# Optimization experiments

Hardware: AMD Instinct MI355X
Metric: run time of the kernel (lower is better)

The kernel has to match this reference:

```python
import jax, jax.numpy as jnp
import numpy as np

N_NODES = 50000
N_EDGES = 800000
IN_FEAT = 256
OUT_FEAT = 256
NUM_RELS = 64
NUM_BASES = 8


def setup_inputs() -> dict:
    key = jax.random.key(0)
    ks = jax.random.split(key, 9)
    x = jax.random.normal(ks[0], (N_NODES, IN_FEAT), dtype=jnp.float32)
    src = jax.random.randint(ks[1], (N_EDGES,), 0, N_NODES, dtype=jnp.int32)
    dst = jax.random.randint(ks[2], (N_EDGES,), 0, N_NODES, dtype=jnp.int32)
    etypes = jax.random.randint(ks[3], (N_EDGES,), 0, NUM_RELS, dtype=jnp.int32)
    norm = jax.random.uniform(ks[4], (N_EDGES, 1), dtype=jnp.float32)
    # glorot-style params
    s_w = (6.0 / (IN_FEAT + OUT_FEAT)) ** 0.5
    weight = jax.random.uniform(ks[5], (NUM_BASES, IN_FEAT, OUT_FEAT), jnp.float32, -s_w, s_w)
    s_c = (6.0 / (NUM_RELS + NUM_BASES)) ** 0.5
    w_comp = jax.random.uniform(ks[6], (NUM_RELS, NUM_BASES), jnp.float32, -s_c, s_c)
    h_bias = jnp.zeros((OUT_FEAT,), jnp.float32)
    loop_weight = jax.random.uniform(ks[7], (IN_FEAT, OUT_FEAT), jnp.float32, -s_w, s_w)
    return {"x": x, "src": src, "dst": dst, "etypes": etypes, "norm": norm,
            "weight": weight, "w_comp": w_comp, "h_bias": h_bias,
            "loop_weight": loop_weight}


def reference(x, src, dst, etypes, norm, weight, w_comp, h_bias, loop_weight):
    # Basis regularizer with num_bases < num_rels:
    #   W_r = sum_b w_comp[r, b] * V_b
    # Per-edge message: msg_e = (x[src_e] @ W_{etype_e}) * norm_e,
    # aggregated by sum onto destination nodes. Since the map is linear,
    # we aggregate per basis first, then apply V_b (8 dense GEMMs).
    n_nodes = x.shape[0]
    coef = w_comp[etypes]                      # [E, B] per-edge basis coeffs
    xs = x[src] * norm                         # [E, D] normalized source feats
    out = jnp.zeros((n_nodes, weight.shape[2]), x.dtype)
    for b in range(weight.shape[0]):           # small fixed loop over bases
        agg = jax.ops.segment_sum(xs * coef[:, b:b + 1], dst,
                                  num_segments=n_nodes)   # [N, D]
        out = out + agg @ weight[b]            # [N, O]
    out = out + h_bias + x @ loop_weight       # bias + self-loop
    return jax.nn.relu(out)
```

## Files before the change

### kernel.cpp

```cpp
#include <hip/hip_runtime.h>
#include <hip/hip_bf16.h>
#include <stdint.h>

#define N_NODES 50000
#define N_EDGES 800000
#define IN_FEAT 256
#define OUT_FEAT 256
#define NUM_RELS 64
#define NUM_BASES 8
#define KTOT 2304
#define KAGG 2048
#define MP 50176
#define NT 36
#define SCAN_BLKS 196

typedef __attribute__((ext_vector_type(8))) __bf16 bf16x8;
typedef __attribute__((ext_vector_type(4))) __bf16 bf16x4;
typedef __attribute__((ext_vector_type(4))) float f32x4;
typedef __attribute__((ext_vector_type(2))) float f32x2;

static __device__ __forceinline__ void gload_lds16(const void* g, void* l) {
  auto gp = (const __attribute__((address_space(1))) void*)(uintptr_t)g;
  auto lp = (__attribute__((address_space(3))) void*)(uint32_t)(uintptr_t)l;
  __builtin_amdgcn_global_load_lds(gp, lp, 16, 0, 0);
}

__global__ void k_prex(const float* __restrict__ x, __bf16* __restrict__ xb) {
  int i = blockIdx.x * 256 + threadIdx.x;
  const float4* xp = (const float4*)x;
  float4 u = xp[i * 2], v = xp[i * 2 + 1];
  bf16x8 o;
  o[0] = (__bf16)u.x; o[1] = (__bf16)u.y; o[2] = (__bf16)u.z; o[3] = (__bf16)u.w;
  o[4] = (__bf16)v.x; o[5] = (__bf16)v.y; o[6] = (__bf16)v.z; o[7] = (__bf16)v.w;
  *(bf16x8*)(xb + (size_t)i * 8) = o;
}

__global__ void k_count(const int* __restrict__ dst, int* __restrict__ deg) {
  int e = blockIdx.x * 256 + threadIdx.x;
  atomicAdd(&deg[dst[e]], 1);
}

__global__ void k_scan1(const int* __restrict__ deg, int* __restrict__ offs,
                        int* __restrict__ bsum) {
  __shared__ int s[256];
  int t = threadIdx.x;
  int i = blockIdx.x * 256 + t;
  int v = (i < N_NODES) ? deg[i] : 0;
  s[t] = v;
  __syncthreads();
  for (int d = 1; d < 256; d <<= 1) {
    int y = (t >= d) ? s[t - d] : 0;
    __syncthreads();
    s[t] += y;
    __syncthreads();
  }
  if (i < N_NODES) offs[i] = s[t] - v;
  if (t == 255) bsum[blockIdx.x] = s[255];
}

__global__ void k_scan3(int* __restrict__ offs, const int* __restrict__ bsum,
                        int* __restrict__ fill) {
  __shared__ int s[256];
  int t = threadIdx.x;
  s[t] = (t < SCAN_BLKS && t < blockIdx.x) ? bsum[t] : 0;
  __syncthreads();
  for (int d = 128; d; d >>= 1) {
    if (t < d) s[t] += s[t + d];
    __syncthreads();
  }
  int base = s[0];
  int i = blockIdx.x * 256 + t;
  if (i < N_NODES) {
    int o = offs[i] + base;
    offs[i] = o;
    fill[i] = o;
  }
}

__global__ void k_scatter(const int* __restrict__ dst, const int* __restrict__ srcv,
                          const int* __restrict__ ety, const float* __restrict__ norm,
                          int* __restrict__ fill, uint2* __restrict__ erec) {
  int e = blockIdx.x * 256 + threadIdx.x;
  int pos = atomicAdd(&fill[dst[e]], 1);
  erec[pos] = make_uint2((unsigned)srcv[e] | ((unsigned)ety[e] << 16),
                         __float_as_uint(norm[e]));
}

#define AGGE(R, XV, ACC)                                                      \
  do {                                                                        \
    int et_ = __builtin_amdgcn_readfirstlane((int)((R).x >> 16));             \
    float nm_ = __uint_as_float((R).y);                                       \
    f32x2 v0_ = {__uint_as_float((XV).x << 16) * nm_,                         \
                 __uint_as_float((XV).x & 0xffff0000u) * nm_};                 \
    f32x2 v1_ = {__uint_as_float((XV).y << 16) * nm_,                         \
                 __uint_as_float((XV).y & 0xffff0000u) * nm_};                 \
    f32x4 cl_ = *(const f32x4*)(w_comp + et_ * 8);                            \
    f32x4 ch_ = *(const f32x4*)(w_comp + et_ * 8 + 4);                        \
    _Pragma("unroll") for (int b = 0; b < 4; ++b) {                           \
      ACC[b][0] += v0_ * cl_[b];                                              \
      ACC[b][1] += v1_ * cl_[b];                                              \
      ACC[b + 4][0] += v0_ * ch_[b];                                          \
      ACC[b + 4][1] += v1_ * ch_[b];                                          \
    }                                                                         \
  } while (0)

#define EDGE4(RP, I, ACC)                                                     \
  do {                                                                        \
    uint2 r0_ = (RP)[(I) + 0], r1_ = (RP)[(I) + 1];                           \
    uint2 r2_ = (RP)[(I) + 2], r3_ = (RP)[(I) + 3];                           \
    uint2 x0_ = *(const uint2*)(xb + (size_t)(r0_.x & 0xffffu) * IN_FEAT + lo4);\
    uint2 x1_ = *(const uint2*)(xb + (size_t)(r1_.x & 0xffffu) * IN_FEAT + lo4);\
    uint2 x2_ = *(const uint2*)(xb + (size_t)(r2_.x & 0xffffu) * IN_FEAT + lo4);\
    uint2 x3_ = *(const uint2*)(xb + (size_t)(r3_.x & 0xffffu) * IN_FEAT + lo4);\
    AGGE(r0_, x0_, ACC); AGGE(r1_, x1_, ACC);                                 \
    AGGE(r2_, x2_, ACC); AGGE(r3_, x3_, ACC);                                 \
  } while (0)

#define EDGE1(RP, I, ACC)                                                     \
  do {                                                                        \
    uint2 r_ = (RP)[(I)];                                                     \
    uint2 x_ = *(const uint2*)(xb + (size_t)(r_.x & 0xffffu) * IN_FEAT + lo4);\
    AGGE(r_, x_, ACC);                                                        \
  } while (0)

__global__ __launch_bounds__(256) void k_agg(
    const __bf16* __restrict__ xb, const float* __restrict__ w_comp,
    const int* __restrict__ offs, const int* __restrict__ fin,
    const uint2* __restrict__ erec, __bf16* __restrict__ A) {
  int t = threadIdx.x;
  int wid = t >> 6, lane = t & 63;
  int na = blockIdx.x * 8 + wid * 2;
  int lo4 = lane * 4;

  f32x2 acca[NUM_BASES][2], accb[NUM_BASES][2];
#pragma unroll
  for (int b = 0; b < NUM_BASES; ++b) {
    acca[b][0] = f32x2{0.f, 0.f}; acca[b][1] = f32x2{0.f, 0.f};
    accb[b][0] = f32x2{0.f, 0.f}; accb[b][1] = f32x2{0.f, 0.f};
  }

  int i0a = __builtin_amdgcn_readfirstlane(offs[na]);
  int ca  = __builtin_amdgcn_readfirstlane(fin[na]) - i0a;
  int i0b = __builtin_amdgcn_readfirstlane(offs[na + 1]);
  int cb  = __builtin_amdgcn_readfirstlane(fin[na + 1]) - i0b;
  const uint2* rpa = erec + i0a;
  const uint2* rpb = erec + i0b;

  int ia = 0, ib = 0;
  int mm = (ca < cb ? ca : cb) & ~3;
  for (; ia < mm; ia += 4, ib += 4) {
    EDGE4(rpa, ia, acca);
    EDGE4(rpb, ib, accb);
  }
  for (; ia + 4 <= ca; ia += 4) EDGE4(rpa, ia, acca);
  for (; ib + 4 <= cb; ib += 4) EDGE4(rpb, ib, accb);
  for (; ia < ca; ++ia) EDGE1(rpa, ia, acca);
  for (; ib < cb; ++ib) EDGE1(rpb, ib, accb);

  __bf16* Ara = A + (size_t)na * KAGG + lo4;
  __bf16* Arb = A + (size_t)(na + 1) * KAGG + lo4;
#pragma unroll
  for (int b = 0; b < NUM_BASES; ++b) {
    bf16x4 oa, ob;
    oa[0] = (__bf16)acca[b][0][0]; oa[1] = (__bf16)acca[b][0][1];
    oa[2] = (__bf16)acca[b][1][0]; oa[3] = (__bf16)acca[b][1][1];
    *(bf16x4*)(Ara + b * 256) = oa;
    ob[0] = (__bf16)accb[b][0][0]; ob[1] = (__bf16)accb[b][0][1];
    ob[2] = (__bf16)accb[b][1][0]; ob[3] = (__bf16)accb[b][1][1];
    *(bf16x4*)(Arb + b * 256) = ob;
  }
}

__global__ void k_prepwf(const float* __restrict__ weight, const float* __restrict__ loop_w,
                         __bf16* __restrict__ Wf) {
  int tid = blockIdx.x * 256 + threadIdx.x;
  int lane6 = tid & 63;
  int F = tid >> 6;
  int kt2 = F >> 4;
  int nf = F & 15;
  int o = nf * 16 + (lane6 & 15);
  int rbase = kt2 * 32 + (lane6 >> 4) * 8;
  bf16x8 v;
#pragma unroll
  for (int j = 0; j < 8; ++j) {
    int r = rbase + j;
    float f = (r < 2048) ? weight[(size_t)r * 256 + o]
                         : loop_w[(size_t)(r - 2048) * 256 + o];
    v[j] = (__bf16)f;
  }
  *(bf16x8*)(Wf + (size_t)tid * 8) = v;
}

__global__ __launch_bounds__(256, 2) void k_gemm(const __bf16* __restrict__ A,
                                                 const __bf16* __restrict__ xb,
                                                 const __bf16* __restrict__ Wf,
                                                 const float* __restrict__ bias,
                                                 float* __restrict__ out) {
  __shared__ __align__(16) __bf16 sA[3 * 64 * 64];

  int t = threadIdx.x;
  int wid = t >> 6, lane = t & 63;
  int tm = blockIdx.x;
  int rfw = __builtin_amdgcn_readfirstlane(wid);

  f32x4 acc[4][4];
#pragma unroll
  for (int m = 0; m < 4; ++m)
#pragma unroll
    for (int n = 0; n < 4; ++n) acc[m][n] = f32x4{0.f, 0.f, 0.f, 0.f};

  int frow = lane & 15;
  int g = lane >> 4;
  int f7 = frow & 7;
  int kb0 = ((g ^ f7) << 4);
  int kb1 = (((4 + g) ^ f7) << 4);

  int rh = t >> 3;
  int qoff = ((t & 7) ^ (rh & 7)) * 8;
  const __bf16* gA[2];
  const __bf16* gX[2];
#pragma unroll
  for (int it = 0; it < 2; ++it) {
    int row = it * 32 + rh;
    gA[it] = A + (size_t)(tm * 64 + row) * KAGG + qoff;
    gX[it] = xb + (size_t)(tm * 64 + row) * IN_FEAT + qoff;
  }
  const __bf16* wfb = Wf + (size_t)(wid * 4) * 512 + lane * 8;

  bf16x8 af[4][2], B0[4][2], B1[4][2];

#define VMWAIT(N) asm volatile("s_waitcnt vmcnt(" #N ")" ::: "memory")
#define BAR()                                       \
  do {                                              \
    asm volatile("" ::: "memory");                  \
    __builtin_amdgcn_s_barrier();                   \
    asm volatile("" ::: "memory");                  \
  } while (0)

#define STAGE(U, BUF)                                                         \
  do {                                                                        \
    char* d_ = (char*)sA + (BUF) * 8192;                                      \
    if ((U) < 32) {                                                           \
      int ko_ = (U) * 64;                                                     \
      gload_lds16(gA[0] + ko_, d_ + rfw * 1024);                              \
      gload_lds16(gA[1] + ko_, d_ + 4096 + rfw * 1024);                       \
    } else {                                                                  \
      int ko_ = ((U) - 32) * 64;                                              \
      gload_lds16(gX[0] + ko_, d_ + rfw * 1024);                              \
      gload_lds16(gX[1] + ko_, d_ + 4096 + rfw * 1024);                       \
    }                                                                         \
  } while (0)

#define LOADB(KT, DST)                                                        \
  do {                                                                        \
    _Pragma("unroll") for (int nf = 0; nf < 4; ++nf) {                        \
      DST[nf][0] = *(const bf16x8*)(wfb + (size_t)(((KT) * 2 + 0) * 16 + nf) * 512); \
      DST[nf][1] = *(const bf16x8*)(wfb + (size_t)(((KT) * 2 + 1) * 16 + nf) * 512); \
    }                                                                         \
  } while (0)

#define READ_A(BUF)                                                           \
  do {                                                                        \
    const char* b_ = (const char*)sA + (BUF) * 8192;                          \
    _Pragma("unroll") for (int mf = 0; mf < 4; ++mf) {                        \
      int r_ = mf * 16 + frow;                                                \
      af[mf][0] = *(const bf16x8*)(b_ + r_ * 128 + kb0);                      \
      af[mf][1] = *(const bf16x8*)(b_ + r_ * 128 + kb1);                      \
    }                                                                         \
  } while (0)

#define MFMA32(BS)                                                            \
  do {                                                                        \
    _Pragma("unroll") for (int mf = 0; mf < 4; ++mf)                          \
    _Pragma("unroll") for (int nf = 0; nf < 4; ++nf) {                        \
      acc[mf][nf] = __builtin_amdgcn_mfma_f32_16x16x32_bf16(                  \
          af[mf][0], BS[nf][0], acc[mf][nf], 0, 0, 0);                        \
      acc[mf][nf] = __builtin_amdgcn_mfma_f32_16x16x32_bf16(                  \
          af[mf][1], BS[nf][1], acc[mf][nf], 0, 0, 0);                        \
    }                                                                         \
  } while (0)

#define STEP(KT, BCUR, BNXT)                                                  \
  do {                                                                        \
    int cb_ = (KT) % 3;                                                       \
    int nb_ = ((KT) + 2) % 3;                                                 \
    int u2_ = ((KT) + 2 < NT) ? (KT) + 2 : NT - 1;                            \
    int un_ = ((KT) + 1 < NT) ? (KT) + 1 : NT - 1;                            \
    LOADB(un_, BNXT);                                                         \
    STAGE(u2_, nb_);                                                          \
    READ_A(cb_);                                                              \
    __builtin_amdgcn_s_setprio(1);                                            \
    MFMA32(BCUR);                                                             \
    __builtin_amdgcn_s_setprio(0);                                            \
    VMWAIT(10);                                                               \
    BAR();                                                                    \
  } while (0)

  LOADB(0, B0);
  STAGE(0, 0);
  STAGE(1, 1);
  VMWAIT(2);
  BAR();

  for (int kt = 0; kt < NT; kt += 2) {
    STEP(kt, B0, B1);
    STEP(kt + 1, B1, B0);
  }
#undef STEP
#undef STAGE
#undef LOADB
#undef READ_A
#undef MFMA32
#undef VMWAIT
#undef BAR

  int r0 = (lane >> 4) * 4;
  int c0 = lane & 15;
#pragma unroll
  for (int m = 0; m < 4; ++m) {
    int rowb = tm * 64 + m * 16 + r0;
#pragma unroll
    for (int n = 0; n < 4; ++n) {
      int col = wid * 64 + n * 16 + c0;
      float bv = bias[col];
#pragma unroll
      for (int r = 0; r < 4; ++r) {
        int row = rowb + r;
        if (row < N_NODES) {
          float v = acc[m][n][r] + bv;
          out[(size_t)row * OUT_FEAT + col] = v > 0.f ? v : 0.f;
        }
      }
    }
  }
}

extern "C" void kernel_launch(void* const* d_in, const int* in_sizes, int n_in,
                              void* d_out, int out_size, void* d_ws, size_t ws_size,
                              hipStream_t stream) {
  const float* x      = (const float*)d_in[0];
  const int*   src    = (const int*)d_in[1];
  const int*   dst    = (const int*)d_in[2];
  const int*   ety    = (const int*)d_in[3];
  const float* norm   = (const float*)d_in[4];
  const float* weight = (const float*)d_in[5];
  const float* w_comp = (const float*)d_in[6];
  const float* h_bias = (const float*)d_in[7];
  const float* loop_w = (const float*)d_in[8];
  float* out = (float*)d_out;

  char* ws = (char*)d_ws;
  __bf16* A  = (__bf16*)ws;
  size_t off = (size_t)MP * KAGG * 2;
  __bf16* xb = (__bf16*)(ws + off);
  off += (size_t)MP * IN_FEAT * 2;
  __bf16* Wf = (__bf16*)(ws + off);
  off += (size_t)256 * KTOT * 2;
  uint2* erec = (uint2*)(ws + off);
  off += (size_t)N_EDGES * 8;
  int* deg   = (int*)(ws + off);
  int* offs  = deg + N_NODES;
  int* fill  = offs + N_NODES;
  int* bsum  = fill + N_NODES;

  hipMemsetAsync(deg, 0, N_NODES * sizeof(int), stream);
  k_prex<<<(N_NODES * IN_FEAT / 8) / 256, 256, 0, stream>>>(x, xb);
  k_count<<<N_EDGES / 256, 256, 0, stream>>>(dst, deg);
  k_scan1<<<SCAN_BLKS, 256, 0, stream>>>(deg, offs, bsum);
  k_scan3<<<SCAN_BLKS, 256, 0, stream>>>(offs, bsum, fill);
  k_scatter<<<N_EDGES / 256, 256, 0, stream>>>(dst, src, ety, norm, fill, erec);
  k_agg<<<N_NODES / 8, 256, 0, stream>>>(xb, w_comp, offs, fill, erec, A);
  k_prepwf<<<288, 256, 0, stream>>>(weight, loop_w, Wf);
  k_gemm<<<MP / 64, 256, 0, stream>>>(A, xb, Wf, h_bias, out);
}
```

Before: 299.9 us.

## Load GEMM A fragments directly from global memory into registers, dropping LDS staging

```diff
diff --git a/kernel.cpp b/kernel.cpp
--- a/kernel.cpp
+++ b/kernel.cpp
@@ -11,19 +11,12 @@
 #define KTOT 2304
 #define KAGG 2048
 #define MP 50176
-#define NT 36
 #define SCAN_BLKS 196
 
 typedef __attribute__((ext_vector_type(8))) __bf16 bf16x8;
 typedef __attribute__((ext_vector_type(4))) __bf16 bf16x4;
 typedef __attribute__((ext_vector_type(4))) float f32x4;
 typedef __attribute__((ext_vector_type(2))) float f32x2;
-
-static __device__ __forceinline__ void gload_lds16(const void* g, void* l) {
-  auto gp = (const __attribute__((address_space(1))) void*)(uintptr_t)g;
-  auto lp = (__attribute__((address_space(3))) void*)(uint32_t)(uintptr_t)l;
-  __builtin_amdgcn_global_load_lds(gp, lp, 16, 0, 0);
-}
 
 __global__ void k_prex(const float* __restrict__ x, __bf16* __restrict__ xb) {
   int i = blockIdx.x * 256 + threadIdx.x;
@@ -196,123 +189,76 @@
                                                  const __bf16* __restrict__ Wf,
                                                  const float* __restrict__ bias,
                                                  float* __restrict__ out) {
-  __shared__ __align__(16) __bf16 sA[3 * 64 * 64];
-
   int t = threadIdx.x;
   int wid = t >> 6, lane = t & 63;
   int tm = blockIdx.x;
-  int rfw = __builtin_amdgcn_readfirstlane(wid);
-
-  f32x4 acc[4][4];
-#pragma unroll
-  for (int m = 0; m < 4; ++m)
-#pragma unroll
-    for (int n = 0; n < 4; ++n) acc[m][n] = f32x4{0.f, 0.f, 0.f, 0.f};
-
   int frow = lane & 15;
   int g = lane >> 4;
-  int f7 = frow & 7;
-  int kb0 = ((g ^ f7) << 4);
-  int kb1 = (((4 + g) ^ f7) << 4);
-
-  int rh = t >> 3;
-  int qoff = ((t & 7) ^ (rh & 7)) * 8;
-  const __bf16* gA[2];
-  const __bf16* gX[2];
-#pragma unroll
-  for (int it = 0; it < 2; ++it) {
-    int row = it * 32 + rh;
-    gA[it] = A + (size_t)(tm * 64 + row) * KAGG + qoff;
-    gX[it] = xb + (size_t)(tm * 64 + row) * IN_FEAT + qoff;
+
+  f32x4 acc[4][4];
+#pragma unroll
+  for (int m = 0; m < 4; ++m)
+#pragma unroll
+    for (int n = 0; n < 4; ++n) acc[m][n] = f32x4{0.f, 0.f, 0.f, 0.f};
+
+  const __bf16* aP[4];
+  const __bf16* xP[4];
+#pragma unroll
+  for (int mf = 0; mf < 4; ++mf) {
+    int row = tm * 64 + mf * 16 + frow;
+    aP[mf] = A + (size_t)row * KAGG + g * 8;
+    xP[mf] = xb + (size_t)row * IN_FEAT + g * 8;
   }
   const __bf16* wfb = Wf + (size_t)(wid * 4) * 512 + lane * 8;
 
-  bf16x8 af[4][2], B0[4][2], B1[4][2];
-
-#define VMWAIT(N) asm volatile("s_waitcnt vmcnt(" #N ")" ::: "memory")
-#define BAR()                                       \
-  do {                                              \
-    asm volatile("" ::: "memory");                  \
-    __builtin_amdgcn_s_barrier();                   \
-    asm volatile("" ::: "memory");                  \
-  } while (0)
-
-#define STAGE(U, BUF)                                                         \
-  do {                                                                        \
-    char* d_ = (char*)sA + (BUF) * 8192;                                      \
-    if ((U) < 32) {                                                           \
-      int ko_ = (U) * 64;                                                     \
-      gload_lds16(gA[0] + ko_, d_ + rfw * 1024);                              \
-      gload_lds16(gA[1] + ko_, d_ + 4096 + rfw * 1024);                       \
+  bf16x8 A0[4], A1[4], A2[4], B0[4], B1[4], B2[4];
+
+#define LD_A(K2, D)                                                           \
+  do {                                                                        \
+    if ((K2) < 64) {                                                          \
+      int ko_ = (K2) * 32;                                                    \
+      _Pragma("unroll") for (int mf = 0; mf < 4; ++mf)                        \
+          D[mf] = *(const bf16x8*)(aP[mf] + ko_);                             \
     } else {                                                                  \
-      int ko_ = ((U) - 32) * 64;                                              \
-      gload_lds16(gX[0] + ko_, d_ + rfw * 1024);                              \
-      gload_lds16(gX[1] + ko_, d_ + 4096 + rfw * 1024);                       \
+      int ko_ = ((K2) - 64) * 32;                                             \
+      _Pragma("unroll") for (int mf = 0; mf < 4; ++mf)                        \
+          D[mf] = *(const bf16x8*)(xP[mf] + ko_);                             \
     }                                                                         \
   } while (0)
 
-#define LOADB(KT, DST)                                                        \
-  do {                                                                        \
-    _Pragma("unroll") for (int nf = 0; nf < 4; ++nf) {                        \
-      DST[nf][0] = *(const bf16x8*)(wfb + (size_t)(((KT) * 2 + 0) * 16 + nf) * 512); \
-      DST[nf][1] = *(const bf16x8*)(wfb + (size_t)(((KT) * 2 + 1) * 16 + nf) * 512); \
-    }                                                                         \
-  } while (0)
-
-#define READ_A(BUF)                                                           \
-  do {                                                                        \
-    const char* b_ = (const char*)sA + (BUF) * 8192;                          \
-    _Pragma("unroll") for (int mf = 0; mf < 4; ++mf) {                        \
-      int r_ = mf * 16 + frow;                                                \
-      af[mf][0] = *(const bf16x8*)(b_ + r_ * 128 + kb0);                      \
-      af[mf][1] = *(const bf16x8*)(b_ + r_ * 128 + kb1);                      \
-    }                                                                         \
-  } while (0)
-
-#define MFMA32(BS)                                                            \
-  do {                                                                        \
+#define LD_B(K2, D)                                                           \
+  do {                                                                        \
+    _Pragma("unroll") for (int nf = 0; nf < 4; ++nf)                          \
+        D[nf] = *(const bf16x8*)(wfb + (size_t)((K2) * 16 + nf) * 512);       \
+  } while (0)
+
+#define FMA16(AS, BS)                                                         \
+  do {                                                                        \
+    __builtin_amdgcn_s_setprio(1);                                            \
     _Pragma("unroll") for (int mf = 0; mf < 4; ++mf)                          \
-    _Pragma("unroll") for (int nf = 0; nf < 4; ++nf) {                        \
-      acc[mf][nf] = __builtin_amdgcn_mfma_f32_16x16x32_bf16(                  \
-          af[mf][0], BS[nf][0], acc[mf][nf], 0, 0, 0);                        \
-      acc[mf][nf] = __builtin_amdgcn_mfma_f32_16x16x32_bf16(                  \
-          af[mf][1], BS[nf][1], acc[mf][nf], 0, 0, 0);                        \
-    }                                                                         \
-  } while (0)
-
-#define STEP(KT, BCUR, BNXT)                                                  \
-  do {                                                                        \
-    int cb_ = (KT) % 3;                                                       \
-    int nb_ = ((KT) + 2) % 3;                                                 \
-    int u2_ = ((KT) + 2 < NT) ? (KT) + 2 : NT - 1;                            \
-    int un_ = ((KT) + 1 < NT) ? (KT) + 1 : NT - 1;                            \
-    LOADB(un_, BNXT);                                                         \
-    STAGE(u2_, nb_);                                                          \
-    READ_A(cb_);                                                              \
-    __builtin_amdgcn_s_setprio(1);                                            \
-    MFMA32(BCUR);                                                             \
+    _Pragma("unroll") for (int nf = 0; nf < 4; ++nf)                          \
+        acc[mf][nf] = __builtin_amdgcn_mfma_f32_16x16x32_bf16(                \
+            AS[mf], BS[nf], acc[mf][nf], 0, 0, 0);                            \
     __builtin_amdgcn_s_setprio(0);                                            \
-    VMWAIT(10);                                                               \
-    BAR();                                                                    \
-  } while (0)
-
-  LOADB(0, B0);
-  STAGE(0, 0);
-  STAGE(1, 1);
-  VMWAIT(2);
-  BAR();
-
-  for (int kt = 0; kt < NT; kt += 2) {
-    STEP(kt, B0, B1);
-    STEP(kt + 1, B1, B0);
-  }
-#undef STEP
-#undef STAGE
-#undef LOADB
-#undef READ_A
-#undef MFMA32
-#undef VMWAIT
-#undef BAR
+  } while (0)
+
+  LD_A(0, A0); LD_B(0, B0);
+  LD_A(1, A1); LD_B(1, B1);
+
+  for (int k = 0; k < 72; k += 3) {
+    int p2 = (k + 2 < 72) ? k + 2 : 71;
+    int p3 = (k + 3 < 72) ? k + 3 : 71;
+    int p4 = (k + 4 < 72) ? k + 4 : 71;
+    LD_A(p2, A2); LD_B(p2, B2);
+    FMA16(A0, B0);
+    LD_A(p3, A0); LD_B(p3, B0);
+    FMA16(A1, B1);
+    LD_A(p4, A1); LD_B(p4, B1);
+    FMA16(A2, B2);
+  }
+#undef LD_A
+#undef LD_B
+#undef FMA16
 
   int r0 = (lane >> 4) * 4;
   int c0 = lane & 15;
```

Measured after the change: 382.7 us. +27.6%, slower.
